# Performance work log

Hardware: AMD Instinct MI355X
Metric: run time of the kernel (lower is better)

The kernel has to match this reference:

```python
import jax, jax.numpy as jnp
import numpy as np

DIM = 4096
N_HEADS = 32
N_KV_HEADS = 8
HEAD_DIM = DIM // N_HEADS  # 128
N_REP = N_HEADS // N_KV_HEADS  # 4
BSZ = 2
SEQLEN = 1024
MAX_SEQ = 1024


def setup_inputs() -> dict:
    key = jax.random.key(0)
    ks = jax.random.split(key, 8)
    x = jax.random.normal(ks[0], (BSZ, SEQLEN, DIM), dtype=jnp.float32)
    # rotary frequencies as cos/sin of the complex freqs_cis
    theta = 10000.0 ** (-jnp.arange(0, HEAD_DIM, 2, dtype=jnp.float32) / HEAD_DIM)  # (64,)
    pos = jnp.arange(SEQLEN, dtype=jnp.float32)
    ang = pos[:, None] * theta[None, :]  # (S, 64)
    freqs_cos = jnp.cos(ang)
    freqs_sin = jnp.sin(ang)
    mask = jnp.zeros((SEQLEN, MAX_SEQ), dtype=jnp.float32)
    input_indexes = jnp.arange(SEQLEN, dtype=jnp.int64) if jax.config.jax_enable_x64 else jnp.arange(SEQLEN, dtype=jnp.int32)
    s = 1.0 / np.sqrt(DIM)
    wq = jax.random.normal(ks[1], (DIM, N_HEADS * HEAD_DIM), dtype=jnp.float32) * s
    wk = jax.random.normal(ks[2], (DIM, N_KV_HEADS * HEAD_DIM), dtype=jnp.float32) * s
    wv = jax.random.normal(ks[3], (DIM, N_KV_HEADS * HEAD_DIM), dtype=jnp.float32) * s
    wo = jax.random.normal(ks[4], (N_HEADS * HEAD_DIM, DIM), dtype=jnp.float32) * s
    cache_k = jnp.zeros((BSZ, MAX_SEQ, N_KV_HEADS, HEAD_DIM), dtype=jnp.float32)
    cache_v = jnp.zeros((BSZ, MAX_SEQ, N_KV_HEADS, HEAD_DIM), dtype=jnp.float32)
    return {"x": x, "freqs_cos": freqs_cos, "freqs_sin": freqs_sin, "mask": mask,
            "input_indexes": input_indexes, "wq": wq, "wk": wk, "wv": wv, "wo": wo,
            "cache_k": cache_k, "cache_v": cache_v}


def _rope(t, cos, sin):
    # t: (B, S, H, D); rotate consecutive (even, odd) pairs as complex mult
    B, S, H, D = t.shape
    tr = t.reshape(B, S, H, D // 2, 2)
    re, im = tr[..., 0], tr[..., 1]
    c = cos[None, :, None, :]
    s = sin[None, :, None, :]
    out_re = re * c - im * s
    out_im = re * s + im * c
    return jnp.stack([out_re, out_im], axis=-1).reshape(B, S, H, D)


def reference(x, freqs_cos, freqs_sin, mask, input_indexes, wq, wk, wv, wo, cache_k, cache_v):
    B, S, _ = x.shape
    xq = (x @ wq).reshape(B, S, N_HEADS, HEAD_DIM)
    xk = (x @ wk).reshape(B, S, N_KV_HEADS, HEAD_DIM)
    xv = (x @ wv).reshape(B, S, N_KV_HEADS, HEAD_DIM)
    xq = _rope(xq, freqs_cos, freqs_sin)
    xk = _rope(xk, freqs_cos, freqs_sin)
    # KV-cache write (index_copy along time dim)
    cache_k = cache_k.at[:, input_indexes].set(xk)
    cache_v = cache_v.at[:, input_indexes].set(xv)
    # GQA attention without materializing repeated KV: group queries per kv head
    q = xq.reshape(B, S, N_KV_HEADS, N_REP, HEAD_DIM)
    scale = 1.0 / np.sqrt(HEAD_DIM)
    # scores: (B, KH, R, S, T)
    scores = jnp.einsum('bsgrd,btgd->bgrst', q, cache_k) * scale
    scores = scores + mask  # mask (S, T) broadcasts
    probs = jax.nn.softmax(scores.astype(jnp.float32), axis=-1).astype(x.dtype)
    out = jnp.einsum('bgrst,btgd->bsgrd', probs, cache_v).reshape(B, S, N_HEADS * HEAD_DIM)
    return out @ wo
```

## Files before the change

kernel.cpp:

```cpp
#include <hip/hip_runtime.h>

typedef unsigned short u16;
typedef __bf16 v8bf __attribute__((ext_vector_type(8)));
typedef float  v4f  __attribute__((ext_vector_type(4)));

static __device__ inline u16 f2bf(float f) {
    unsigned int u = __float_as_uint(f);
    unsigned int r = u + 0x7fff + ((u >> 16) & 1);
    return (u16)(r >> 16);
}

static __device__ __forceinline__ void gl2lds(const u16* g, u16* l) {
    __builtin_amdgcn_global_load_lds(
        (const __attribute__((address_space(1))) void*)g,
        (__attribute__((address_space(3))) void*)l,
        16, 0, 0);
}

#define S_BARRIER() __builtin_amdgcn_s_barrier()
#define MFMA16(a, b, c) __builtin_amdgcn_mfma_f32_16x16x32_bf16((a), (b), (c), 0, 0, 0)

__global__ __launch_bounds__(256)
void cvt_kernel(const float* __restrict__ in, u16* __restrict__ out) {
    size_t i = ((size_t)blockIdx.x * 256 + threadIdx.x) * 8;
    float4 a = *(const float4*)&in[i];
    float4 b = *(const float4*)&in[i + 4];
    ushort4 lo, hi;
    lo.x = f2bf(a.x); lo.y = f2bf(a.y); lo.z = f2bf(a.z); lo.w = f2bf(a.w);
    hi.x = f2bf(b.x); hi.y = f2bf(b.y); hi.z = f2bf(b.z); hi.w = f2bf(b.w);
    *(ushort4*)&out[i] = lo;
    *(ushort4*)&out[i + 4] = hi;
}

__global__ __launch_bounds__(256)
void transpose_cvt_kernel(const float* __restrict__ w, u16* __restrict__ wt,
                          int N, int K) {
    __shared__ __attribute__((aligned(16))) u16 Ts[64][72];
    const int k0 = blockIdx.y * 64, n0 = blockIdx.x * 64;
    const int t = threadIdx.x;
    const int rk = t >> 4, cn = (t & 15) * 4;
    #pragma unroll
    for (int p = 0; p < 4; p++) {
        float4 v = *(const float4*)&w[(size_t)(k0 + rk + p * 16) * N + n0 + cn];
        Ts[cn + 0][rk + p * 16] = f2bf(v.x);
        Ts[cn + 1][rk + p * 16] = f2bf(v.y);
        Ts[cn + 2][rk + p * 16] = f2bf(v.z);
        Ts[cn + 3][rk + p * 16] = f2bf(v.w);
    }
    __syncthreads();
    const int n = t >> 3, kc = (t & 7) * 8;
    #pragma unroll
    for (int p = 0; p < 2; p++)
        *(uint4*)&wt[(size_t)(n0 + n + p * 32) * K + k0 + kc] =
            *(const uint4*)&Ts[n + p * 32][kc];
}

template<int BSUB>
__device__ __forceinline__ void gemm_core(
    const u16* __restrict__ A, const u16* __restrict__ Bt, int K,
    int m0, int n0, u16* LDSp, v4f (&acc)[4][BSUB / 4]) {

    constexpr int ASUB = 8;
    constexpr int NJ   = BSUB / 4;
    constexpr int BPW  = BSUB / 8;
    constexpr int BUFE = (ASUB + BSUB) * 512;

    const int tid  = threadIdx.x;
    const int w    = tid >> 6;
    const int lane = tid & 63;
    const int quad = lane >> 4;
    const int l16  = lane & 15;
    const int wmb  = (w >> 2) * 4;
    const int wnb  = (w & 3) * NJ;
    const int srow = lane >> 2;
    const int scol = ((lane & 3) * 8) ^ ((lane & 32) ? 16 : 0);
    const int roff = l16 * 32 + ((quad * 8) ^ ((l16 & 8) << 1));

    const size_t aoff = (size_t)(m0 + w * 16 + srow) * K + scol;
    size_t boff[BPW];
    #pragma unroll
    for (int q = 0; q < BPW; q++)
        boff[q] = (size_t)(n0 + (w * BPW + q) * 16 + srow) * K + scol;

    const int NT = K >> 5;

    #pragma unroll
    for (int i = 0; i < 4; i++)
        #pragma unroll
        for (int j = 0; j < NJ; j++)
            acc[i][j] = v4f{0.f, 0.f, 0.f, 0.f};

    #pragma unroll
    for (int p = 0; p < 3; p++) {
        u16* buf = LDSp + p * BUFE;
        const size_t ko = (size_t)p * 32;
        gl2lds(&A[aoff + ko], buf + w * 512);
        #pragma unroll
        for (int q = 0; q < BPW; q++)
            gl2lds(&Bt[boff[q] + ko], buf + (ASUB + w * BPW + q) * 512);
    }
    if constexpr (BPW == 3) { asm volatile("s_waitcnt vmcnt(8)" ::: "memory"); }
    else                    { asm volatile("s_waitcnt vmcnt(6)" ::: "memory"); }
    S_BARRIER();

    for (int t = 0; t < NT; ++t) {
        const u16* Ac = LDSp + (size_t)(t & 3) * BUFE;
        u16* An = LDSp + (size_t)((t + 3) & 3) * BUFE;
        const size_t kn = (size_t)((t + 3 < NT) ? t + 3 : 0) * 32;

        v8bf a0, a1, b[NJ];

        #pragma unroll
        for (int j = 0; j < NJ; j++)
            b[j] = *(const v8bf*)&Ac[((ASUB + wnb + j) << 9) + roff];
        a0 = *(const v8bf*)&Ac[((wmb + 0) << 9) + roff];
        a1 = *(const v8bf*)&Ac[((wmb + 1) << 9) + roff];
        gl2lds(&A[aoff + kn], An + w * 512);
        S_BARRIER();
        __builtin_amdgcn_s_setprio(1);
        #pragma unroll
        for (int j = 0; j < NJ; j++) {
            acc[0][j] = MFMA16(a0, b[j], acc[0][j]);
            acc[1][j] = MFMA16(a1, b[j], acc[1][j]);
        }
        __builtin_amdgcn_s_setprio(0);
        S_BARRIER();

        a0 = *(const v8bf*)&Ac[((wmb + 2) << 9) + roff];
        a1 = *(const v8bf*)&Ac[((wmb + 3) << 9) + roff];
        #pragma unroll
        for (int q = 0; q < BPW; q++)
            gl2lds(&Bt[boff[q] + kn], An + (ASUB + w * BPW + q) * 512);
        S_BARRIER();
        __builtin_amdgcn_s_setprio(1);
        #pragma unroll
        for (int j = 0; j < NJ; j++) {
            acc[2][j] = MFMA16(a0, b[j], acc[2][j]);
            acc[3][j] = MFMA16(a1, b[j], acc[3][j]);
        }
        __builtin_amdgcn_s_setprio(0);
        if constexpr (BPW == 3) { asm volatile("s_waitcnt vmcnt(8)" ::: "memory"); }
        else                    { asm volatile("s_waitcnt vmcnt(6)" ::: "memory"); }
        S_BARRIER();
    }
}

__global__ __launch_bounds__(512, 2)
void gemm_qkv(const u16* __restrict__ A, const u16* __restrict__ Bt,
              u16* __restrict__ qb, u16* __restrict__ kout, u16* __restrict__ vt,
              const float* __restrict__ fcos, const float* __restrict__ fsin,
              int K) {
    __shared__ __attribute__((aligned(16))) u16 LDSp[4 * 32 * 512];
    const int m0 = blockIdx.y * 128;
    const int n0 = blockIdx.x * 384;

    v4f acc[4][6];
    gemm_core<24>(A, Bt, K, m0, n0, LDSp, acc);

    const int tid  = threadIdx.x;
    const int w    = tid >> 6;
    const int lane = tid & 63;
    const int quad = lane >> 4;
    const int l16  = lane & 15;
    const int wm   = (w >> 2) * 64;
    const int wn   = (w & 3) * 96;
    const bool odd = l16 & 1;

    #pragma unroll
    for (int i = 0; i < 4; i++) {
        #pragma unroll
        for (int j = 0; j < 6; j++) {
            const int fcol0 = n0 + wn + j * 16;
            const int col   = fcol0 + l16;
            const int row0  = m0 + wm + i * 16 + quad * 4;
            const bool isV = fcol0 >= 5120;
            const bool isK = (fcol0 >= 4096) && !isV;
            if (isV) {
                const int gd = col - 5120;
                const int b  = row0 >> 10, tt = row0 & 1023;
                ushort4 o;
                o.x = f2bf(acc[i][j][0]); o.y = f2bf(acc[i][j][1]);
                o.z = f2bf(acc[i][j][2]); o.w = f2bf(acc[i][j][3]);
                *(ushort4*)&vt[(size_t)b * 1048576 + (size_t)gd * 1024 + tt] = o;
            } else {
                u16* outp = isK ? kout : qb;
                const int ldc   = isK ? 1024 : 4096;
                const int cbase = isK ? 4096 : 0;
                const int ii = (col & 127) >> 1;
                #pragma unroll
                for (int r = 0; r < 4; r++) {
                    float val = acc[i][j][r];
                    float other = __shfl_xor(val, 1);
                    int s = (row0 + r) & 1023;
                    float c  = fcos[s * 64 + ii];
                    float sn = fsin[s * 64 + ii];
                    float o = odd ? fmaf(other, sn, val * c)
                                  : fmaf(val, c, -(other * sn));
                    outp[(size_t)(row0 + r) * ldc + (col - cbase)] = f2bf(o);
                }
            }
        }
    }
}

__global__ __launch_bounds__(512, 2)
void gemm_wo(const u16* __restrict__ A, const u16* __restrict__ Bt,
             float* __restrict__ C, int M, int N, int K) {
    __shared__ __attribute__((aligned(16))) u16 LDSp[4 * 24 * 512];
    const int m0 = blockIdx.y * 128;
    const int n0 = blockIdx.x * 256;

    v4f acc[4][4];
    gemm_core<16>(A, Bt, K, m0, n0, LDSp, acc);

    const int tid  = threadIdx.x;
    const int w    = tid >> 6;
    const int lane = tid & 63;
    const int quad = lane >> 4;
    const int l16  = lane & 15;
    const int wm   = (w >> 2) * 64;
    const int wn   = (w & 3) * 64;

    #pragma unroll
    for (int i = 0; i < 4; i++)
        #pragma unroll
        for (int j = 0; j < 4; j++) {
            const int col  = n0 + wn + j * 16 + l16;
            const int row0 = m0 + wm + i * 16 + quad * 4;
            #pragma unroll
            for (int r = 0; r < 4; r++)
                C[(size_t)(row0 + r) * N + col] = acc[i][j][r];
        }
}

__global__ __launch_bounds__(256)
void attn_kernel(const u16* __restrict__ q, const u16* __restrict__ k,
                 const u16* __restrict__ vt, u16* __restrict__ out) {
    __shared__ __attribute__((aligned(16))) u16 Qs[64 * 136];
    __shared__ __attribute__((aligned(16))) u16 Ks[64 * 136];
    __shared__ __attribute__((aligned(16))) u16 Vs[128 * 72];
    __shared__ __attribute__((aligned(16))) u16 Ps[4 * 16 * 72];

    const int tid  = threadIdx.x;
    const int qt   = blockIdx.x;
    const int bh   = blockIdx.y;
    const int b    = bh >> 5;
    const int h    = bh & 31;
    const int g    = h >> 2;
    const int wave = tid >> 6, lane = tid & 63, quad = lane >> 4, l16 = lane & 15;
    const int wq0  = wave * 16;
    const int g8   = tid & 15;
    const int trow = tid >> 4;

    const size_t qbase = ((size_t)b * 1024) * 4096 + (size_t)h * 128;
    const size_t kbase = ((size_t)b * 1024) * 1024 + (size_t)g * 128;
    const size_t vtb   = (size_t)b * 1048576 + (size_t)g * 131072;
    const float kscale = 0.08838834764831845f * 1.4426950408889634f;

    #pragma unroll
    for (int p = 0; p < 4; p++) {
        int r = trow + p * 16;
        *(uint4*)&Qs[r * 136 + g8 * 8] =
            *(const uint4*)&q[qbase + (size_t)(qt * 64 + r) * 4096 + g8 * 8];
    }

    float l_run[4] = {0.f, 0.f, 0.f, 0.f};
    v4f O[8];
    #pragma unroll
    for (int df = 0; df < 8; df++) O[df] = v4f{0.f, 0.f, 0.f, 0.f};

    u16* Pw = &Ps[wave * 16 * 72];

    for (int t0 = 0; t0 < 1024; t0 += 64) {
        __syncthreads();
        #pragma unroll
        for (int p = 0; p < 4; p++) {
            int r = trow + p * 16;
            *(uint4*)&Ks[r * 136 + g8 * 8] =
                *(const uint4*)&k[kbase + (size_t)(t0 + r) * 1024 + g8 * 8];
        }
        #pragma unroll
        for (int p = 0; p < 4; p++) {
            int d = (tid >> 3) + p * 32;
            int toff = (tid & 7) * 8;
            *(uint4*)&Vs[d * 72 + toff] =
                *(const uint4*)&vt[vtb + (size_t)d * 1024 + t0 + toff];
        }
        __syncthreads();

        v4f sfrag[4];
        #pragma unroll
        for (int jn = 0; jn < 4; jn++) sfrag[jn] = v4f{0.f, 0.f, 0.f, 0.f};
        #pragma unroll
        for (int ks = 0; ks < 4; ks++) {
            v8bf af = *(const v8bf*)&Qs[(wq0 + l16) * 136 + ks * 32 + quad * 8];
            #pragma unroll
            for (int jn = 0; jn < 4; jn++) {
                v8bf bf = *(const v8bf*)&Ks[(jn * 16 + l16) * 136 + ks * 32 + quad * 8];
                sfrag[jn] = __builtin_amdgcn_mfma_f32_16x16x32_bf16(af, bf, sfrag[jn], 0, 0, 0);
            }
        }

        #pragma unroll
        for (int jn = 0; jn < 4; jn++)
            #pragma unroll
            for (int r = 0; r < 4; r++) {
                float pv = __builtin_amdgcn_exp2f(sfrag[jn][r] * kscale);
                l_run[r] += pv;
                Pw[(quad * 4 + r) * 72 + jn * 16 + l16] = f2bf(pv);
            }

        #pragma unroll
        for (int ts = 0; ts < 2; ts++) {
            v8bf pf = *(const v8bf*)&Pw[l16 * 72 + ts * 32 + quad * 8];
            #pragma unroll
            for (int df = 0; df < 8; df++) {
                v8bf vf = *(const v8bf*)&Vs[(df * 16 + l16) * 72 + ts * 32 + quad * 8];
                O[df] = __builtin_amdgcn_mfma_f32_16x16x32_bf16(pf, vf, O[df], 0, 0, 0);
            }
        }
    }

    #pragma unroll
    for (int off = 1; off < 16; off <<= 1)
        #pragma unroll
        for (int r = 0; r < 4; r++)
            l_run[r] += __shfl_xor(l_run[r], off, 64);
    float inv[4];
    #pragma unroll
    for (int r = 0; r < 4; r++) inv[r] = __builtin_amdgcn_rcpf(l_run[r]);

    const size_t obase = ((size_t)b * 1024 + qt * 64 + wq0 + quad * 4) * 4096 + (size_t)h * 128;
    #pragma unroll
    for (int df = 0; df < 8; df++)
        #pragma unroll
        for (int r = 0; r < 4; r++)
            out[obase + (size_t)r * 4096 + df * 16 + l16] = f2bf(O[df][r] * inv[r]);
}

extern "C" void kernel_launch(void* const* d_in, const int* in_sizes, int n_in,
                              void* d_out, int out_size, void* d_ws, size_t ws_size,
                              hipStream_t stream) {
    const float* x    = (const float*)d_in[0];
    const float* fcos = (const float*)d_in[1];
    const float* fsin = (const float*)d_in[2];
    const float* wq   = (const float*)d_in[5];
    const float* wk   = (const float*)d_in[6];
    const float* wv   = (const float*)d_in[7];
    const float* wo   = (const float*)d_in[8];

    u16* xb = (u16*)d_ws;
    u16* Wt = xb + (size_t)2048 * 4096;
    u16* qb = Wt + (size_t)6144 * 4096;
    u16* kb = qb + (size_t)2048 * 4096;
    u16* vb = kb + (size_t)2048 * 1024;
    u16* ab = xb;

    dim3 blk(256);
    cvt_kernel<<<dim3(4096), blk, 0, stream>>>(x, xb);
    transpose_cvt_kernel<<<dim3(64, 64), blk, 0, stream>>>(wq, Wt, 4096, 4096);
    transpose_cvt_kernel<<<dim3(16, 64), blk, 0, stream>>>(wk, Wt + (size_t)4096 * 4096, 1024, 4096);
    transpose_cvt_kernel<<<dim3(16, 64), blk, 0, stream>>>(wv, Wt + (size_t)5120 * 4096, 1024, 4096);
    gemm_qkv<<<dim3(16, 16), dim3(512), 0, stream>>>(xb, Wt, qb, kb, vb, fcos, fsin, 4096);
    attn_kernel<<<dim3(16, 64), blk, 0, stream>>>(qb, kb, vb, ab);
    transpose_cvt_kernel<<<dim3(64, 64), blk, 0, stream>>>(wo, Wt, 4096, 4096);
    gemm_wo<<<dim3(16, 16), dim3(512), 0, stream>>>(ab, Wt, (float*)d_out, 2048, 4096, 4096);
}
```

Before: 481.0 us.

## Halve GEMM N-tiles, triple-buffer LDS, and raise occupancy to four blocks

Both projection GEMMs now use half-width N tiles (192 for QKV, 128 for Wo), which doubles the grid to 512 blocks. The LDS ring drops from four to three stages, rotated by pointer swap, with a two-ahead prefetch and matching vmcnt waits. Launch bounds ask for four blocks per CU, so the aim is more resident waves and better CU coverage on a 256-CU part instead of only 256 large tiles. In exchange, arithmetic intensity per tile drops and there is less prefetch depth to hide latency.

Result: no change. 489.9 us (+1.8%).

```diff
diff --git a/kernel.cpp b/kernel.cpp
--- a/kernel.cpp
+++ b/kernel.cpp
@@ -55,15 +55,13 @@
             *(const uint4*)&Ts[n + p * 32][kc];
 }
 
-template<int BSUB>
+template<int BN16, int SLOTS>
 __device__ __forceinline__ void gemm_core(
     const u16* __restrict__ A, const u16* __restrict__ Bt, int K,
-    int m0, int n0, u16* LDSp, v4f (&acc)[4][BSUB / 4]) {
-
-    constexpr int ASUB = 8;
-    constexpr int NJ   = BSUB / 4;
-    constexpr int BPW  = BSUB / 8;
-    constexpr int BUFE = (ASUB + BSUB) * 512;
+    int m0, int n0, u16* LDSp, v4f (&acc)[4][BN16 / 4]) {
+
+    constexpr int NJ   = BN16 / 4;
+    constexpr int BUFE = (8 + BN16) * 512;
 
     const int tid  = threadIdx.x;
     const int w    = tid >> 6;
@@ -76,11 +74,10 @@
     const int scol = ((lane & 3) * 8) ^ ((lane & 32) ? 16 : 0);
     const int roff = l16 * 32 + ((quad * 8) ^ ((l16 & 8) << 1));
 
-    const size_t aoff = (size_t)(m0 + w * 16 + srow) * K + scol;
-    size_t boff[BPW];
-    #pragma unroll
-    for (int q = 0; q < BPW; q++)
-        boff[q] = (size_t)(n0 + (w * BPW + q) * 16 + srow) * K + scol;
+    const size_t g0 = (size_t)(m0 + w * 16 + srow) * K + scol;
+    const size_t g1 = (size_t)(n0 + w * 16 + srow) * K + scol;
+    const size_t g2 = (size_t)(n0 + (8 + (w & 3)) * 16 + srow) * K + scol;
+    const int   l0 = w, l1 = 8 + w, l2 = 16 + (w & 3);
 
     const int NT = K >> 5;
 
@@ -90,32 +87,35 @@
         for (int j = 0; j < NJ; j++)
             acc[i][j] = v4f{0.f, 0.f, 0.f, 0.f};
 
-    #pragma unroll
-    for (int p = 0; p < 3; p++) {
-        u16* buf = LDSp + p * BUFE;
+    u16* b0p = LDSp;
+    u16* b1p = LDSp + BUFE;
+    u16* b2p = LDSp + 2 * BUFE;
+
+    #pragma unroll
+    for (int p = 0; p < 2; p++) {
+        u16* buf = p ? b1p : b0p;
         const size_t ko = (size_t)p * 32;
-        gl2lds(&A[aoff + ko], buf + w * 512);
-        #pragma unroll
-        for (int q = 0; q < BPW; q++)
-            gl2lds(&Bt[boff[q] + ko], buf + (ASUB + w * BPW + q) * 512);
-    }
-    if constexpr (BPW == 3) { asm volatile("s_waitcnt vmcnt(8)" ::: "memory"); }
-    else                    { asm volatile("s_waitcnt vmcnt(6)" ::: "memory"); }
+        gl2lds(&A[g0 + ko],  buf + l0 * 512);
+        gl2lds(&Bt[g1 + ko], buf + l1 * 512);
+        if constexpr (SLOTS == 3) gl2lds(&Bt[g2 + ko], buf + l2 * 512);
+    }
+    if constexpr (SLOTS == 3) { asm volatile("s_waitcnt vmcnt(3)" ::: "memory"); }
+    else                      { asm volatile("s_waitcnt vmcnt(2)" ::: "memory"); }
     S_BARRIER();
 
     for (int t = 0; t < NT; ++t) {
-        const u16* Ac = LDSp + (size_t)(t & 3) * BUFE;
-        u16* An = LDSp + (size_t)((t + 3) & 3) * BUFE;
-        const size_t kn = (size_t)((t + 3 < NT) ? t + 3 : 0) * 32;
+        const u16* Ac = b0p;
+        u16* An = b2p;
+        const size_t kn = (size_t)((t + 2 < NT) ? t + 2 : 0) * 32;
 
         v8bf a0, a1, b[NJ];
 
         #pragma unroll
         for (int j = 0; j < NJ; j++)
-            b[j] = *(const v8bf*)&Ac[((ASUB + wnb + j) << 9) + roff];
+            b[j] = *(const v8bf*)&Ac[((8 + wnb + j) << 9) + roff];
         a0 = *(const v8bf*)&Ac[((wmb + 0) << 9) + roff];
         a1 = *(const v8bf*)&Ac[((wmb + 1) << 9) + roff];
-        gl2lds(&A[aoff + kn], An + w * 512);
+        gl2lds(&A[g0 + kn], An + l0 * 512);
         S_BARRIER();
         __builtin_amdgcn_s_setprio(1);
         #pragma unroll
@@ -128,9 +128,8 @@
 
         a0 = *(const v8bf*)&Ac[((wmb + 2) << 9) + roff];
         a1 = *(const v8bf*)&Ac[((wmb + 3) << 9) + roff];
-        #pragma unroll
-        for (int q = 0; q < BPW; q++)
-            gl2lds(&Bt[boff[q] + kn], An + (ASUB + w * BPW + q) * 512);
+        gl2lds(&Bt[g1 + kn], An + l1 * 512);
+        if constexpr (SLOTS == 3) gl2lds(&Bt[g2 + kn], An + l2 * 512);
         S_BARRIER();
         __builtin_amdgcn_s_setprio(1);
         #pragma unroll
@@ -139,23 +138,25 @@
             acc[3][j] = MFMA16(a1, b[j], acc[3][j]);
         }
         __builtin_amdgcn_s_setprio(0);
-        if constexpr (BPW == 3) { asm volatile("s_waitcnt vmcnt(8)" ::: "memory"); }
-        else                    { asm volatile("s_waitcnt vmcnt(6)" ::: "memory"); }
+        if constexpr (SLOTS == 3) { asm volatile("s_waitcnt vmcnt(3)" ::: "memory"); }
+        else                      { asm volatile("s_waitcnt vmcnt(2)" ::: "memory"); }
         S_BARRIER();
-    }
-}
-
-__global__ __launch_bounds__(512, 2)
+
+        u16* tmp = b0p; b0p = b1p; b1p = b2p; b2p = tmp;
+    }
+}
+
+__global__ __launch_bounds__(512, 4)
 void gemm_qkv(const u16* __restrict__ A, const u16* __restrict__ Bt,
               u16* __restrict__ qb, u16* __restrict__ kout, u16* __restrict__ vt,
               const float* __restrict__ fcos, const float* __restrict__ fsin,
               int K) {
-    __shared__ __attribute__((aligned(16))) u16 LDSp[4 * 32 * 512];
+    __shared__ __attribute__((aligned(16))) u16 LDSp[3 * 20 * 512];
     const int m0 = blockIdx.y * 128;
-    const int n0 = blockIdx.x * 384;
-
-    v4f acc[4][6];
-    gemm_core<24>(A, Bt, K, m0, n0, LDSp, acc);
+    const int n0 = blockIdx.x * 192;
+
+    v4f acc[4][3];
+    gemm_core<12, 3>(A, Bt, K, m0, n0, LDSp, acc);
 
     const int tid  = threadIdx.x;
     const int w    = tid >> 6;
@@ -163,13 +164,13 @@
     const int quad = lane >> 4;
     const int l16  = lane & 15;
     const int wm   = (w >> 2) * 64;
-    const int wn   = (w & 3) * 96;
+    const int wn   = (w & 3) * 48;
     const bool odd = l16 & 1;
 
     #pragma unroll
     for (int i = 0; i < 4; i++) {
         #pragma unroll
-        for (int j = 0; j < 6; j++) {
+        for (int j = 0; j < 3; j++) {
             const int fcol0 = n0 + wn + j * 16;
             const int col   = fcol0 + l16;
             const int row0  = m0 + wm + i * 16 + quad * 4;
@@ -203,15 +204,15 @@
     }
 }
 
-__global__ __launch_bounds__(512, 2)
+__global__ __launch_bounds__(512, 4)
 void gemm_wo(const u16* __restrict__ A, const u16* __restrict__ Bt,
              float* __restrict__ C, int M, int N, int K) {
-    __shared__ __attribute__((aligned(16))) u16 LDSp[4 * 24 * 512];
+    __shared__ __attribute__((aligned(16))) u16 LDSp[3 * 16 * 512];
     const int m0 = blockIdx.y * 128;
-    const int n0 = blockIdx.x * 256;
-
-    v4f acc[4][4];
-    gemm_core<16>(A, Bt, K, m0, n0, LDSp, acc);
+    const int n0 = blockIdx.x * 128;
+
+    v4f acc[4][2];
+    gemm_core<8, 2>(A, Bt, K, m0, n0, LDSp, acc);
 
     const int tid  = threadIdx.x;
     const int w    = tid >> 6;
@@ -219,12 +220,12 @@
     const int quad = lane >> 4;
     const int l16  = lane & 15;
     const int wm   = (w >> 2) * 64;
-    const int wn   = (w & 3) * 64;
+    const int wn   = (w & 3) * 32;
 
     #pragma unroll
     for (int i = 0; i < 4; i++)
         #pragma unroll
-        for (int j = 0; j < 4; j++) {
+        for (int j = 0; j < 2; j++) {
             const int col  = n0 + wn + j * 16 + l16;
             const int row0 = m0 + wm + i * 16 + quad * 4;
             #pragma unroll
@@ -361,8 +362,8 @@
     transpose_cvt_kernel<<<dim3(64, 64), blk, 0, stream>>>(wq, Wt, 4096, 4096);
     transpose_cvt_kernel<<<dim3(16, 64), blk, 0, stream>>>(wk, Wt + (size_t)4096 * 4096, 1024, 4096);
     transpose_cvt_kernel<<<dim3(16, 64), blk, 0, stream>>>(wv, Wt + (size_t)5120 * 4096, 1024, 4096);
-    gemm_qkv<<<dim3(16, 16), dim3(512), 0, stream>>>(xb, Wt, qb, kb, vb, fcos, fsin, 4096);
+    gemm_qkv<<<dim3(32, 16), dim3(512), 0, stream>>>(xb, Wt, qb, kb, vb, fcos, fsin, 4096);
     attn_kernel<<<dim3(16, 64), blk, 0, stream>>>(qb, kb, vb, ab);
     transpose_cvt_kernel<<<dim3(64, 64), blk, 0, stream>>>(wo, Wt, 4096, 4096);
-    gemm_wo<<<dim3(16, 16), dim3(512), 0, stream>>>(ab, Wt, (float*)d_out, 2048, 4096, 4096);
-}
+    gemm_wo<<<dim3(32, 16), dim3(512), 0, stream>>>(ab, Wt, (float*)d_out, 2048, 4096, 4096);
+}
```
